# Kernel tuning notes

Measured on AMD Instinct MI355X. Metric: run time of the kernel, lower is better.

## Reference

```python
import jax, jax.numpy as jnp
import numpy as np

B, S, D, F = 8, 4096, 512, 4

def setup_inputs() -> dict:
    key = jax.random.key(0)
    k1, k2, k3, k4 = jax.random.split(key, 4)
    return {
        "inputs": jax.random.normal(k1, (B, S, D), dtype=jnp.float32),
        "values": jax.random.normal(k2, (B, S, F * D), dtype=jnp.float32),
        "W_out": jax.random.normal(k3, (2 * D, D), dtype=jnp.float32) * 0.02,
        "w_score": jax.random.normal(k4, (D, 1), dtype=jnp.float32) * 0.02,
        "b_score": jnp.zeros((1,), dtype=jnp.float32),
        "n": F,
    }

def reference(inputs, values, W_out, w_score, b_score, n):
    # inputs: [B,S,D]; values: [B,S,F*D] -> per-position lattice factors [B,S,F,D]
    b, s, d = inputs.shape
    f = values.shape[2] // d
    mem = values.reshape(b, s, f, d)
    # dot-attention of each position's query over its F factor vectors
    scores = jnp.einsum('bsd,bsfd->bsf', inputs, mem)  # [B,S,F]
    valid = jnp.arange(f) < n                          # lattice mask from n
    scores = jnp.where(valid, scores, jnp.float32(-1e9))
    attn = jax.nn.softmax(scores, axis=-1)
    ctx = jnp.einsum('bsf,bsfd->bsd', attn, mem)       # [B,S,D]
    # OpenNMT GlobalAttention (dot): tanh(linear_out([ctx; q])), no bias
    cat = jnp.concatenate([ctx, inputs], axis=-1)      # [B,S,2D]
    attn_h = jnp.tanh(cat @ W_out)                     # [B,S,D]
    # sigmoid context gate from the query
    gate = jax.nn.sigmoid(inputs @ w_score + b_score)  # [B,S,1]
    # dropout is identity in eval; residual add
    return attn_h * gate + inputs
```

## Files before the change

### kernel.cpp

```cpp
#include <hip/hip_runtime.h>
#include <hip/hip_bf16.h>
#include <math.h>

#define BATCH 8
#define SEQ   4096
#define DIM   512
#define FDIM  4
#define M_TOTAL (BATCH*SEQ)
#define K_TOTAL (2*DIM)
#define N_TOTAL DIM

#define PRE_BLOCKS (M_TOTAL/4)
#define WCONV_BLOCKS ((K_TOTAL/64)*(N_TOTAL/64))

typedef __bf16 bf16x8 __attribute__((ext_vector_type(8)));
typedef float  f32x4  __attribute__((ext_vector_type(4)));

__device__ __forceinline__ void gload_lds16(const void* g, void* l) {
    __builtin_amdgcn_global_load_lds(
        (__attribute__((address_space(1))) void*)(void*)g,
        (__attribute__((address_space(3))) void*)l,
        16, 0, 0);
}

__device__ __forceinline__ float dot4(float4 a, float4 b) {
    return a.x*b.x + a.y*b.y + a.z*b.z + a.w*b.w;
}

__device__ __forceinline__ void store_bf4(__hip_bfloat16* dst, float4 v) {
    __hip_bfloat16 t[4];
    t[0] = __float2bfloat16(v.x); t[1] = __float2bfloat16(v.y);
    t[2] = __float2bfloat16(v.z); t[3] = __float2bfloat16(v.w);
    *reinterpret_cast<uint2*>(dst) = *reinterpret_cast<const uint2*>(t);
}

__device__ __forceinline__ float fast_tanh(float x) {
    float e = __expf(2.f * x);
    return 1.f - 2.f * __builtin_amdgcn_rcpf(e + 1.f);
}

__global__ __launch_bounds__(256)
void pre_kernel(const float* __restrict__ inputs,
                const float* __restrict__ values,
                const float* __restrict__ W,
                const float* __restrict__ w_score,
                const float* __restrict__ b_score,
                const int*   __restrict__ n_ptr,
                __hip_bfloat16* __restrict__ cat,
                float* __restrict__ gate,
                __hip_bfloat16* __restrict__ Wt)
{
    __shared__ float ws[64][65];

    const int tid  = threadIdx.x;

    if (blockIdx.x >= PRE_BLOCKS) {
        const int t  = blockIdx.x - PRE_BLOCKS;
        const int k0 = (t & 15) * 64;
        const int n0 = (t >> 4) * 64;
        #pragma unroll
        for (int i = 0; i < 16; ++i) {
            int e = i * 256 + tid;
            int r = e >> 6, c = e & 63;
            ws[r][c] = W[(size_t)(k0 + r) * N_TOTAL + n0 + c];
        }
        __syncthreads();
        #pragma unroll
        for (int i = 0; i < 16; ++i) {
            int e = i * 256 + tid;
            int nr = e >> 6, kc = e & 63;
            Wt[(size_t)(n0 + nr) * K_TOTAL + k0 + kc] = __float2bfloat16(ws[kc][nr]);
        }
        return;
    }

    const int lane = tid & 63;
    const int wv   = tid >> 6;
    const int p    = blockIdx.x * 4 + wv;

    const float4* qg = (const float4*)(inputs + (size_t)p * DIM);
    float4 qa = qg[lane], qb = qg[lane + 64];

    const float4* vg = (const float4*)(values + (size_t)p * (FDIM*DIM));
    float4 ma[4], mb[4];
    float s[4];
    #pragma unroll
    for (int f = 0; f < 4; ++f) {
        ma[f] = vg[f * 128 + lane];
        mb[f] = vg[f * 128 + lane + 64];
        s[f] = dot4(qa, ma[f]) + dot4(qb, mb[f]);
    }
    const float4* wg = (const float4*)w_score;
    float g = dot4(qa, wg[lane]) + dot4(qb, wg[lane + 64]);

    #pragma unroll
    for (int off = 1; off < 64; off <<= 1) {
        s[0] += __shfl_xor(s[0], off, 64);
        s[1] += __shfl_xor(s[1], off, 64);
        s[2] += __shfl_xor(s[2], off, 64);
        s[3] += __shfl_xor(s[3], off, 64);
        g    += __shfl_xor(g,    off, 64);
    }

    const int nv = *n_ptr;
    #pragma unroll
    for (int f = 0; f < 4; ++f) if (f >= nv) s[f] = -1e9f;
    float mx = fmaxf(fmaxf(s[0], s[1]), fmaxf(s[2], s[3]));
    float e0 = __expf(s[0] - mx), e1 = __expf(s[1] - mx);
    float e2 = __expf(s[2] - mx), e3 = __expf(s[3] - mx);
    float inv = __builtin_amdgcn_rcpf(e0 + e1 + e2 + e3);
    float a[4] = { e0 * inv, e1 * inv, e2 * inv, e3 * inv };

    float4 ca = {0.f, 0.f, 0.f, 0.f}, cb = {0.f, 0.f, 0.f, 0.f};
    #pragma unroll
    for (int f = 0; f < 4; ++f) {
        ca.x += a[f] * ma[f].x; ca.y += a[f] * ma[f].y;
        ca.z += a[f] * ma[f].z; ca.w += a[f] * ma[f].w;
        cb.x += a[f] * mb[f].x; cb.y += a[f] * mb[f].y;
        cb.z += a[f] * mb[f].z; cb.w += a[f] * mb[f].w;
    }

    __hip_bfloat16* cp = cat + (size_t)p * K_TOTAL;
    store_bf4(cp +        4 * lane, ca);
    store_bf4(cp + 256  + 4 * lane, cb);
    store_bf4(cp + 512  + 4 * lane, qa);
    store_bf4(cp + 768  + 4 * lane, qb);

    if (lane == 0) {
        float t = g + b_score[0];
        gate[p] = __builtin_amdgcn_rcpf(1.f + __expf(-t));
    }
}

__global__ __launch_bounds__(256)
void gemm_ep(const __hip_bfloat16* __restrict__ A,
             const __hip_bfloat16* __restrict__ Bt,
             const float* __restrict__ gate,
             const float* __restrict__ inputs,
             float* __restrict__ out)
{
    __shared__ __align__(16) __hip_bfloat16 As[128 * 64];
    __shared__ __align__(16) __hip_bfloat16 Bs[128 * 64];

    const int tid  = threadIdx.x;
    const int bm   = blockIdx.x;
    const int bn   = blockIdx.y;
    const int wid  = tid >> 6;
    const int lane = tid & 63;
    const int wr   = wid >> 1;
    const int wc   = wid & 1;
    const int la   = lane & 15;
    const int lb   = lane >> 4;

    const int K = K_TOTAL;
    const __hip_bfloat16* Ag = A  + (size_t)(bm * 128) * K;
    const __hip_bfloat16* Bg = Bt + (size_t)(bn * 128) * K;

    f32x4 acc[4][4] = {};

    for (int kt = 0; kt < K; kt += 64) {
        __syncthreads();
        #pragma unroll
        for (int ps = 0; ps < 4; ++ps) {
            int cl  = ps * 256 + tid;
            int row = cl >> 3;
            int c   = cl & 7;
            int sc_ = c ^ (row & 7);
            gload_lds16(Ag + (size_t)row * K + kt + sc_ * 8, As + cl * 8);
            gload_lds16(Bg + (size_t)row * K + kt + sc_ * 8, Bs + cl * 8);
        }
        __syncthreads();

        #pragma unroll
        for (int kk = 0; kk < 2; ++kk) {
            bf16x8 af[4], bfv[4];
            #pragma unroll
            for (int i = 0; i < 4; ++i) {
                int row = wr * 64 + i * 16 + la;
                int c   = (kk * 4 + lb) ^ (row & 7);
                af[i] = *reinterpret_cast<const bf16x8*>(As + row * 64 + c * 8);
            }
            #pragma unroll
            for (int j = 0; j < 4; ++j) {
                int row = wc * 64 + j * 16 + la;
                int c   = (kk * 4 + lb) ^ (row & 7);
                bfv[j] = *reinterpret_cast<const bf16x8*>(Bs + row * 64 + c * 8);
            }
            #pragma unroll
            for (int i = 0; i < 4; ++i)
                #pragma unroll
                for (int j = 0; j < 4; ++j)
                    acc[i][j] = __builtin_amdgcn_mfma_f32_16x16x32_bf16(af[i], bfv[j], acc[i][j], 0, 0, 0);
        }
    }

    const int row0 = bm * 128 + wr * 64;
    const int col0 = bn * 128 + wc * 64;
    #pragma unroll
    for (int i = 0; i < 4; ++i) {
        #pragma unroll
        for (int j = 0; j < 4; ++j) {
            const int col = col0 + j * 16 + la;
            const int rb  = row0 + i * 16 + lb * 4;
            #pragma unroll
            for (int r = 0; r < 4; ++r) {
                const int row = rb + r;
                float v = fast_tanh(acc[i][j][r]) * gate[row] + inputs[(size_t)row * DIM + col];
                out[(size_t)row * DIM + col] = v;
            }
        }
    }
}

extern "C" void kernel_launch(void* const* d_in, const int* in_sizes, int n_in,
                              void* d_out, int out_size, void* d_ws, size_t ws_size,
                              hipStream_t stream) {
    const float* inputs  = (const float*)d_in[0];
    const float* values  = (const float*)d_in[1];
    const float* W_out   = (const float*)d_in[2];
    const float* w_score = (const float*)d_in[3];
    const float* b_score = (const float*)d_in[4];
    const int*   n_ptr   = (const int*)d_in[5];
    float* out = (float*)d_out;

    char* ws = (char*)d_ws;
    __hip_bfloat16* cat  = (__hip_bfloat16*)ws;
    float*          gate = (float*)(ws + (size_t)M_TOTAL * K_TOTAL * 2);
    __hip_bfloat16* Wt   = (__hip_bfloat16*)(ws + (size_t)M_TOTAL * K_TOTAL * 2
                                                + (size_t)M_TOTAL * 4);

    pre_kernel<<<PRE_BLOCKS + WCONV_BLOCKS, 256, 0, stream>>>(
        inputs, values, W_out, w_score, b_score, n_ptr, cat, gate, Wt);
    dim3 g3(M_TOTAL / 128, N_TOTAL / 128);
    gemm_ep<<<g3, 256, 0, stream>>>(cat, Wt, gate, inputs, out);
}
```

Measured before the change: 135.3 us.

## Stop materializing query half of cat; convert fp32 inputs to bf16 inside GEMM

The pre-kernel now writes only the bf16 context (half the previous buffer) instead of the full [ctx; q] concatenation. For the second half of K, the GEMM loads fp32 inputs directly, converts them to bf16 in registers and stores them into the swizzled LDS tile. This removes a write and re-read of the query half, but the GEMM now reads fp32 (twice the bytes) through synchronous register loads rather than async global_load_lds, and each input tile is re-read by the four N-blocks. Launch bounds also add a min-blocks hint of 4.

```diff
diff --git a/kernel.cpp b/kernel.cpp
--- a/kernel.cpp
+++ b/kernel.cpp
@@ -46,7 +46,7 @@
                 const float* __restrict__ w_score,
                 const float* __restrict__ b_score,
                 const int*   __restrict__ n_ptr,
-                __hip_bfloat16* __restrict__ cat,
+                __hip_bfloat16* __restrict__ ctx,
                 float* __restrict__ gate,
                 __hip_bfloat16* __restrict__ Wt)
 {
@@ -120,11 +120,9 @@
         cb.z += a[f] * mb[f].z; cb.w += a[f] * mb[f].w;
     }
 
-    __hip_bfloat16* cp = cat + (size_t)p * K_TOTAL;
+    __hip_bfloat16* cp = ctx + (size_t)p * DIM;
     store_bf4(cp +        4 * lane, ca);
     store_bf4(cp + 256  + 4 * lane, cb);
-    store_bf4(cp + 512  + 4 * lane, qa);
-    store_bf4(cp + 768  + 4 * lane, qb);
 
     if (lane == 0) {
         float t = g + b_score[0];
@@ -132,8 +130,8 @@
     }
 }
 
-__global__ __launch_bounds__(256)
-void gemm_ep(const __hip_bfloat16* __restrict__ A,
+__global__ __launch_bounds__(256, 4)
+void gemm_ep(const __hip_bfloat16* __restrict__ Actx,
              const __hip_bfloat16* __restrict__ Bt,
              const float* __restrict__ gate,
              const float* __restrict__ inputs,
@@ -152,22 +150,42 @@
     const int la   = lane & 15;
     const int lb   = lane >> 4;
 
-    const int K = K_TOTAL;
-    const __hip_bfloat16* Ag = A  + (size_t)(bm * 128) * K;
-    const __hip_bfloat16* Bg = Bt + (size_t)(bn * 128) * K;
+    const __hip_bfloat16* Ag = Actx + (size_t)(bm * 128) * DIM;
+    const float*          Qg = inputs + (size_t)(bm * 128) * DIM;
+    const __hip_bfloat16* Bg = Bt + (size_t)(bn * 128) * K_TOTAL;
 
     f32x4 acc[4][4] = {};
 
-    for (int kt = 0; kt < K; kt += 64) {
+    for (int kt = 0; kt < K_TOTAL; kt += 64) {
         __syncthreads();
-        #pragma unroll
-        for (int ps = 0; ps < 4; ++ps) {
-            int cl  = ps * 256 + tid;
-            int row = cl >> 3;
-            int c   = cl & 7;
-            int sc_ = c ^ (row & 7);
-            gload_lds16(Ag + (size_t)row * K + kt + sc_ * 8, As + cl * 8);
-            gload_lds16(Bg + (size_t)row * K + kt + sc_ * 8, Bs + cl * 8);
+        if (kt < 512) {
+            #pragma unroll
+            for (int ps = 0; ps < 4; ++ps) {
+                int cl  = ps * 256 + tid;
+                int row = cl >> 3;
+                int c   = cl & 7;
+                int sc_ = c ^ (row & 7);
+                gload_lds16(Ag + (size_t)row * DIM + kt + sc_ * 8, As + cl * 8);
+                gload_lds16(Bg + (size_t)row * K_TOTAL + kt + sc_ * 8, Bs + cl * 8);
+            }
+        } else {
+            #pragma unroll
+            for (int ps = 0; ps < 4; ++ps) {
+                int cl  = ps * 256 + tid;
+                int row = cl >> 3;
+                int c   = cl & 7;
+                int sc_ = c ^ (row & 7);
+                gload_lds16(Bg + (size_t)row * K_TOTAL + kt + sc_ * 8, Bs + cl * 8);
+                const float* src = Qg + (size_t)row * DIM + (kt - 512) + sc_ * 8;
+                float4 f0 = ((const float4*)src)[0];
+                float4 f1 = ((const float4*)src)[1];
+                __hip_bfloat16 t[8];
+                t[0] = __float2bfloat16(f0.x); t[1] = __float2bfloat16(f0.y);
+                t[2] = __float2bfloat16(f0.z); t[3] = __float2bfloat16(f0.w);
+                t[4] = __float2bfloat16(f1.x); t[5] = __float2bfloat16(f1.y);
+                t[6] = __float2bfloat16(f1.z); t[7] = __float2bfloat16(f1.w);
+                *reinterpret_cast<uint4*>(As + cl * 8) = *reinterpret_cast<const uint4*>(t);
+            }
         }
         __syncthreads();
 
@@ -224,13 +242,13 @@
     float* out = (float*)d_out;
 
     char* ws = (char*)d_ws;
-    __hip_bfloat16* cat  = (__hip_bfloat16*)ws;
-    float*          gate = (float*)(ws + (size_t)M_TOTAL * K_TOTAL * 2);
-    __hip_bfloat16* Wt   = (__hip_bfloat16*)(ws + (size_t)M_TOTAL * K_TOTAL * 2
+    __hip_bfloat16* ctx  = (__hip_bfloat16*)ws;
+    float*          gate = (float*)(ws + (size_t)M_TOTAL * DIM * 2);
+    __hip_bfloat16* Wt   = (__hip_bfloat16*)(ws + (size_t)M_TOTAL * DIM * 2
                                                 + (size_t)M_TOTAL * 4);
 
     pre_kernel<<<PRE_BLOCKS + WCONV_BLOCKS, 256, 0, stream>>>(
-        inputs, values, W_out, w_score, b_score, n_ptr, cat, gate, Wt);
+        inputs, values, W_out, w_score, b_score, n_ptr, ctx, gate, Wt);
     dim3 g3(M_TOTAL / 128, N_TOTAL / 128);
-    gemm_ep<<<g3, 256, 0, stream>>>(cat, Wt, gate, inputs, out);
-}
+    gemm_ep<<<g3, 256, 0, stream>>>(ctx, Wt, gate, inputs, out);
+}
```

Result: faster. 126.9 us (-6.2%).

## Enlarge GEMM tiles to 256x256 with double-buffered LDS and bf16 residual

Applied to the files above, without the earlier changes.

The GEMM now uses 256x256 tiles with 512 threads and double-buffers its LDS stages, so global-to-LDS loads overlap the MFMA work through manual waitcnt and barriers. Block indices are swizzled for better L2 locality, and gate values are cached in LDS. The residual now reads the bf16 copy of the query from the cat buffer instead of the fp32 inputs, which cuts epilogue bandwidth but adds bf16 rounding error to the residual term. Larger tiles give fewer blocks (256), which may reduce occupancy and raise register pressure.

```diff
diff --git a/kernel.cpp b/kernel.cpp
--- a/kernel.cpp
+++ b/kernel.cpp
@@ -12,6 +12,11 @@
 
 #define PRE_BLOCKS (M_TOTAL/4)
 #define WCONV_BLOCKS ((K_TOTAL/64)*(N_TOTAL/64))
+
+#define BM 256
+#define BN 256
+#define BK 64
+#define NKT (K_TOTAL/BK)
 
 typedef __bf16 bf16x8 __attribute__((ext_vector_type(8)));
 typedef float  f32x4  __attribute__((ext_vector_type(4)));
@@ -132,72 +137,96 @@
     }
 }
 
-__global__ __launch_bounds__(256)
+__global__ __launch_bounds__(512, 2)
 void gemm_ep(const __hip_bfloat16* __restrict__ A,
              const __hip_bfloat16* __restrict__ Bt,
              const float* __restrict__ gate,
-             const float* __restrict__ inputs,
              float* __restrict__ out)
 {
-    __shared__ __align__(16) __hip_bfloat16 As[128 * 64];
-    __shared__ __align__(16) __hip_bfloat16 Bs[128 * 64];
-
-    const int tid  = threadIdx.x;
-    const int bm   = blockIdx.x;
-    const int bn   = blockIdx.y;
+    __shared__ __align__(16) __hip_bfloat16 As[2][BM * BK];
+    __shared__ __align__(16) __hip_bfloat16 Bs[2][BN * BK];
+    __shared__ float gateLds[BM];
+
+    const int tid = threadIdx.x;
+    const int logical = (blockIdx.x & 7) * 32 + (blockIdx.x >> 3);
+    const int bm = logical >> 1;
+    const int bn = logical & 1;
+
     const int wid  = tid >> 6;
     const int lane = tid & 63;
-    const int wr   = wid >> 1;
-    const int wc   = wid & 1;
+    const int wr   = wid & 1;
+    const int wc   = wid >> 1;
     const int la   = lane & 15;
     const int lb   = lane >> 4;
 
-    const int K = K_TOTAL;
-    const __hip_bfloat16* Ag = A  + (size_t)(bm * 128) * K;
-    const __hip_bfloat16* Bg = Bt + (size_t)(bn * 128) * K;
-
-    f32x4 acc[4][4] = {};
-
-    for (int kt = 0; kt < K; kt += 64) {
-        __syncthreads();
+    const __hip_bfloat16* Ag = A  + (size_t)(bm * BM) * K_TOTAL;
+    const __hip_bfloat16* Bg = Bt + (size_t)(bn * BN) * K_TOTAL;
+
+    if (tid < BM) gateLds[tid] = gate[bm * BM + tid];
+    __syncthreads();
+
+    auto STAGE = [&](int t, int buf) {
+        const int kt = t * BK;
         #pragma unroll
         for (int ps = 0; ps < 4; ++ps) {
-            int cl  = ps * 256 + tid;
+            int cl  = ps * 512 + tid;
             int row = cl >> 3;
             int c   = cl & 7;
-            int sc_ = c ^ (row & 7);
-            gload_lds16(Ag + (size_t)row * K + kt + sc_ * 8, As + cl * 8);
-            gload_lds16(Bg + (size_t)row * K + kt + sc_ * 8, Bs + cl * 8);
-        }
-        __syncthreads();
-
+            int sc  = c ^ (row & 7);
+            gload_lds16(Ag + (size_t)row * K_TOTAL + kt + sc * 8, &As[buf][cl * 8]);
+            gload_lds16(Bg + (size_t)row * K_TOTAL + kt + sc * 8, &Bs[buf][cl * 8]);
+        }
+    };
+
+    f32x4 acc[8][4] = {};
+
+    auto COMPUTE = [&](int buf) {
         #pragma unroll
         for (int kk = 0; kk < 2; ++kk) {
-            bf16x8 af[4], bfv[4];
-            #pragma unroll
-            for (int i = 0; i < 4; ++i) {
-                int row = wr * 64 + i * 16 + la;
-                int c   = (kk * 4 + lb) ^ (row & 7);
-                af[i] = *reinterpret_cast<const bf16x8*>(As + row * 64 + c * 8);
+            bf16x8 af[8], bfv[4];
+            #pragma unroll
+            for (int i = 0; i < 8; ++i) {
+                int row = wr * 128 + i * 16 + la;
+                int cc  = (kk * 4 + lb) ^ (row & 7);
+                af[i] = *reinterpret_cast<const bf16x8*>(&As[buf][row * BK + cc * 8]);
             }
             #pragma unroll
             for (int j = 0; j < 4; ++j) {
                 int row = wc * 64 + j * 16 + la;
-                int c   = (kk * 4 + lb) ^ (row & 7);
-                bfv[j] = *reinterpret_cast<const bf16x8*>(Bs + row * 64 + c * 8);
+                int cc  = (kk * 4 + lb) ^ (row & 7);
+                bfv[j] = *reinterpret_cast<const bf16x8*>(&Bs[buf][row * BK + cc * 8]);
             }
             #pragma unroll
-            for (int i = 0; i < 4; ++i)
+            for (int i = 0; i < 8; ++i)
                 #pragma unroll
                 for (int j = 0; j < 4; ++j)
                     acc[i][j] = __builtin_amdgcn_mfma_f32_16x16x32_bf16(af[i], bfv[j], acc[i][j], 0, 0, 0);
         }
-    }
-
-    const int row0 = bm * 128 + wr * 64;
-    const int col0 = bn * 128 + wc * 64;
-    #pragma unroll
-    for (int i = 0; i < 4; ++i) {
+    };
+
+    STAGE(0, 0);
+    STAGE(1, 1);
+
+    #pragma unroll 2
+    for (int t = 0; t < NKT - 2; ++t) {
+        asm volatile("s_waitcnt vmcnt(8)" ::: "memory");
+        __builtin_amdgcn_s_barrier();
+        COMPUTE(t & 1);
+        asm volatile("s_waitcnt lgkmcnt(0)" ::: "memory");
+        __builtin_amdgcn_s_barrier();
+        STAGE(t + 2, t & 1);
+    }
+    asm volatile("s_waitcnt vmcnt(8)" ::: "memory");
+    __builtin_amdgcn_s_barrier();
+    COMPUTE(0);
+    asm volatile("s_waitcnt vmcnt(0)" ::: "memory");
+    __builtin_amdgcn_s_barrier();
+    COMPUTE(1);
+
+    const int row0 = bm * BM + wr * 128;
+    const int col0 = bn * BN + wc * 64;
+    #pragma unroll
+    for (int i = 0; i < 8; ++i) {
         #pragma unroll
         for (int j = 0; j < 4; ++j) {
             const int col = col0 + j * 16 + la;
@@ -205,7 +234,8 @@
             #pragma unroll
             for (int r = 0; r < 4; ++r) {
                 const int row = rb + r;
-                float v = fast_tanh(acc[i][j][r]) * gate[row] + inputs[(size_t)row * DIM + col];
+                float q = __bfloat162float(A[(size_t)row * K_TOTAL + 512 + col]);
+                float v = fast_tanh(acc[i][j][r]) * gateLds[row - bm * BM] + q;
                 out[(size_t)row * DIM + col] = v;
             }
         }
@@ -231,6 +261,5 @@
 
     pre_kernel<<<PRE_BLOCKS + WCONV_BLOCKS, 256, 0, stream>>>(
         inputs, values, W_out, w_score, b_score, n_ptr, cat, gate, Wt);
-    dim3 g3(M_TOTAL / 128, N_TOTAL / 128);
-    gemm_ep<<<g3, 256, 0, stream>>>(cat, Wt, gate, inputs, out);
-}
+    gemm_ep<<<(M_TOTAL / BM) * (N_TOTAL / BN), 512, 0, stream>>>(cat, Wt, gate, out);
+}
```

After: 140.9 us. +4.2%, slower.

## Fuse attention preprocessing into GEMM with per-block LDS cat tile

Applied to the files above, without the earlier changes.

Each block computes softmax context, gate and the bf16 concatenated row tile for 32 positions directly into swizzled LDS, then runs the MFMA GEMM over the full N=512 against the transposed weight read from global/L2 with register double-buffering. The epilogue takes the residual from the LDS copy of the query. This removes the global cat/gate workspace round trip and the separate inputs reread. In exchange, every block streams the whole weight matrix from L2, and the residual is rounded to bf16.

```diff
diff --git a/kernel.cpp b/kernel.cpp
--- a/kernel.cpp
+++ b/kernel.cpp
@@ -10,18 +10,12 @@
 #define K_TOTAL (2*DIM)
 #define N_TOTAL DIM
 
-#define PRE_BLOCKS (M_TOTAL/4)
+#define MB 32
+#define FUSED_BLOCKS (M_TOTAL/MB)
 #define WCONV_BLOCKS ((K_TOTAL/64)*(N_TOTAL/64))
 
 typedef __bf16 bf16x8 __attribute__((ext_vector_type(8)));
 typedef float  f32x4  __attribute__((ext_vector_type(4)));
-
-__device__ __forceinline__ void gload_lds16(const void* g, void* l) {
-    __builtin_amdgcn_global_load_lds(
-        (__attribute__((address_space(1))) void*)(void*)g,
-        (__attribute__((address_space(3))) void*)l,
-        16, 0, 0);
-}
 
 __device__ __forceinline__ float dot4(float4 a, float4 b) {
     return a.x*b.x + a.y*b.y + a.z*b.z + a.w*b.w;
@@ -40,176 +34,170 @@
 }
 
 __global__ __launch_bounds__(256)
-void pre_kernel(const float* __restrict__ inputs,
-                const float* __restrict__ values,
-                const float* __restrict__ W,
-                const float* __restrict__ w_score,
-                const float* __restrict__ b_score,
-                const int*   __restrict__ n_ptr,
-                __hip_bfloat16* __restrict__ cat,
-                float* __restrict__ gate,
-                __hip_bfloat16* __restrict__ Wt)
+void wconv(const float* __restrict__ W, __hip_bfloat16* __restrict__ Wt)
 {
     __shared__ float ws[64][65];
+    const int tid = threadIdx.x;
+    const int t  = blockIdx.x;
+    const int k0 = (t & 15) * 64;
+    const int n0 = (t >> 4) * 64;
+    #pragma unroll
+    for (int i = 0; i < 16; ++i) {
+        int e = i * 256 + tid;
+        int r = e >> 6, c = e & 63;
+        ws[r][c] = W[(size_t)(k0 + r) * N_TOTAL + n0 + c];
+    }
+    __syncthreads();
+    #pragma unroll
+    for (int i = 0; i < 16; ++i) {
+        int e = i * 256 + tid;
+        int nr = e >> 6, kc = e & 63;
+        Wt[(size_t)(n0 + nr) * K_TOTAL + k0 + kc] = __float2bfloat16(ws[kc][nr]);
+    }
+}
+
+__device__ __forceinline__ void cat_store4(__hip_bfloat16* catL, int row, int k, float4 v) {
+    int ck   = k >> 3;
+    int phys = ck ^ (row & 7);
+    char* dst = (char*)catL + row * 2048 + (phys << 4) + ((k & 7) << 1);
+    store_bf4((__hip_bfloat16*)dst, v);
+}
+
+__global__ __launch_bounds__(256, 2)
+void fused_kernel(const float* __restrict__ inputs,
+                  const float* __restrict__ values,
+                  const __hip_bfloat16* __restrict__ Bt,
+                  const float* __restrict__ w_score,
+                  const float* __restrict__ b_score,
+                  const int*   __restrict__ n_ptr,
+                  float* __restrict__ out)
+{
+    __shared__ __align__(16) __hip_bfloat16 catL[MB * K_TOTAL];
+    __shared__ float gateL[MB];
 
     const int tid  = threadIdx.x;
-
-    if (blockIdx.x >= PRE_BLOCKS) {
-        const int t  = blockIdx.x - PRE_BLOCKS;
-        const int k0 = (t & 15) * 64;
-        const int n0 = (t >> 4) * 64;
-        #pragma unroll
-        for (int i = 0; i < 16; ++i) {
-            int e = i * 256 + tid;
-            int r = e >> 6, c = e & 63;
-            ws[r][c] = W[(size_t)(k0 + r) * N_TOTAL + n0 + c];
-        }
-        __syncthreads();
-        #pragma unroll
-        for (int i = 0; i < 16; ++i) {
-            int e = i * 256 + tid;
-            int nr = e >> 6, kc = e & 63;
-            Wt[(size_t)(n0 + nr) * K_TOTAL + k0 + kc] = __float2bfloat16(ws[kc][nr]);
-        }
-        return;
-    }
-
     const int lane = tid & 63;
     const int wv   = tid >> 6;
-    const int p    = blockIdx.x * 4 + wv;
-
-    const float4* qg = (const float4*)(inputs + (size_t)p * DIM);
-    float4 qa = qg[lane], qb = qg[lane + 64];
-
-    const float4* vg = (const float4*)(values + (size_t)p * (FDIM*DIM));
-    float4 ma[4], mb[4];
-    float s[4];
-    #pragma unroll
-    for (int f = 0; f < 4; ++f) {
-        ma[f] = vg[f * 128 + lane];
-        mb[f] = vg[f * 128 + lane + 64];
-        s[f] = dot4(qa, ma[f]) + dot4(qb, mb[f]);
-    }
+    const int bp   = blockIdx.x * MB;
+    const int nv   = *n_ptr;
+
     const float4* wg = (const float4*)w_score;
-    float g = dot4(qa, wg[lane]) + dot4(qb, wg[lane + 64]);
-
-    #pragma unroll
-    for (int off = 1; off < 64; off <<= 1) {
-        s[0] += __shfl_xor(s[0], off, 64);
-        s[1] += __shfl_xor(s[1], off, 64);
-        s[2] += __shfl_xor(s[2], off, 64);
-        s[3] += __shfl_xor(s[3], off, 64);
-        g    += __shfl_xor(g,    off, 64);
-    }
-
-    const int nv = *n_ptr;
-    #pragma unroll
-    for (int f = 0; f < 4; ++f) if (f >= nv) s[f] = -1e9f;
-    float mx = fmaxf(fmaxf(s[0], s[1]), fmaxf(s[2], s[3]));
-    float e0 = __expf(s[0] - mx), e1 = __expf(s[1] - mx);
-    float e2 = __expf(s[2] - mx), e3 = __expf(s[3] - mx);
-    float inv = __builtin_amdgcn_rcpf(e0 + e1 + e2 + e3);
-    float a[4] = { e0 * inv, e1 * inv, e2 * inv, e3 * inv };
-
-    float4 ca = {0.f, 0.f, 0.f, 0.f}, cb = {0.f, 0.f, 0.f, 0.f};
-    #pragma unroll
-    for (int f = 0; f < 4; ++f) {
-        ca.x += a[f] * ma[f].x; ca.y += a[f] * ma[f].y;
-        ca.z += a[f] * ma[f].z; ca.w += a[f] * ma[f].w;
-        cb.x += a[f] * mb[f].x; cb.y += a[f] * mb[f].y;
-        cb.z += a[f] * mb[f].z; cb.w += a[f] * mb[f].w;
-    }
-
-    __hip_bfloat16* cp = cat + (size_t)p * K_TOTAL;
-    store_bf4(cp +        4 * lane, ca);
-    store_bf4(cp + 256  + 4 * lane, cb);
-    store_bf4(cp + 512  + 4 * lane, qa);
-    store_bf4(cp + 768  + 4 * lane, qb);
-
-    if (lane == 0) {
-        float t = g + b_score[0];
-        gate[p] = __builtin_amdgcn_rcpf(1.f + __expf(-t));
-    }
-}
-
-__global__ __launch_bounds__(256)
-void gemm_ep(const __hip_bfloat16* __restrict__ A,
-             const __hip_bfloat16* __restrict__ Bt,
-             const float* __restrict__ gate,
-             const float* __restrict__ inputs,
-             float* __restrict__ out)
-{
-    __shared__ __align__(16) __hip_bfloat16 As[128 * 64];
-    __shared__ __align__(16) __hip_bfloat16 Bs[128 * 64];
-
-    const int tid  = threadIdx.x;
-    const int bm   = blockIdx.x;
-    const int bn   = blockIdx.y;
-    const int wid  = tid >> 6;
-    const int lane = tid & 63;
-    const int wr   = wid >> 1;
-    const int wc   = wid & 1;
-    const int la   = lane & 15;
-    const int lb   = lane >> 4;
-
-    const int K = K_TOTAL;
-    const __hip_bfloat16* Ag = A  + (size_t)(bm * 128) * K;
-    const __hip_bfloat16* Bg = Bt + (size_t)(bn * 128) * K;
-
-    f32x4 acc[4][4] = {};
-
-    for (int kt = 0; kt < K; kt += 64) {
-        __syncthreads();
-        #pragma unroll
-        for (int ps = 0; ps < 4; ++ps) {
-            int cl  = ps * 256 + tid;
-            int row = cl >> 3;
-            int c   = cl & 7;
-            int sc_ = c ^ (row & 7);
-            gload_lds16(Ag + (size_t)row * K + kt + sc_ * 8, As + cl * 8);
-            gload_lds16(Bg + (size_t)row * K + kt + sc_ * 8, Bs + cl * 8);
-        }
-        __syncthreads();
-
-        #pragma unroll
-        for (int kk = 0; kk < 2; ++kk) {
-            bf16x8 af[4], bfv[4];
-            #pragma unroll
-            for (int i = 0; i < 4; ++i) {
-                int row = wr * 64 + i * 16 + la;
-                int c   = (kk * 4 + lb) ^ (row & 7);
-                af[i] = *reinterpret_cast<const bf16x8*>(As + row * 64 + c * 8);
-            }
-            #pragma unroll
-            for (int j = 0; j < 4; ++j) {
-                int row = wc * 64 + j * 16 + la;
-                int c   = (kk * 4 + lb) ^ (row & 7);
-                bfv[j] = *reinterpret_cast<const bf16x8*>(Bs + row * 64 + c * 8);
-            }
-            #pragma unroll
-            for (int i = 0; i < 4; ++i)
-                #pragma unroll
-                for (int j = 0; j < 4; ++j)
-                    acc[i][j] = __builtin_amdgcn_mfma_f32_16x16x32_bf16(af[i], bfv[j], acc[i][j], 0, 0, 0);
-        }
-    }
-
-    const int row0 = bm * 128 + wr * 64;
-    const int col0 = bn * 128 + wc * 64;
-    #pragma unroll
-    for (int i = 0; i < 4; ++i) {
-        #pragma unroll
-        for (int j = 0; j < 4; ++j) {
-            const int col = col0 + j * 16 + la;
-            const int rb  = row0 + i * 16 + lb * 4;
+    #pragma unroll 2
+    for (int it = 0; it < MB / 4; ++it) {
+        const int p = wv * (MB / 4) + it;
+        const float4* qg = (const float4*)(inputs + (size_t)(bp + p) * DIM);
+        float4 qa = qg[lane], qb = qg[lane + 64];
+
+        const float4* vg = (const float4*)(values + (size_t)(bp + p) * (FDIM*DIM));
+        float4 ma[4], mb[4];
+        float s[4];
+        #pragma unroll
+        for (int f = 0; f < 4; ++f) {
+            ma[f] = vg[f * 128 + lane];
+            mb[f] = vg[f * 128 + lane + 64];
+            s[f] = dot4(qa, ma[f]) + dot4(qb, mb[f]);
+        }
+        float g = dot4(qa, wg[lane]) + dot4(qb, wg[lane + 64]);
+
+        #pragma unroll
+        for (int off = 1; off < 64; off <<= 1) {
+            s[0] += __shfl_xor(s[0], off, 64);
+            s[1] += __shfl_xor(s[1], off, 64);
+            s[2] += __shfl_xor(s[2], off, 64);
+            s[3] += __shfl_xor(s[3], off, 64);
+            g    += __shfl_xor(g,    off, 64);
+        }
+
+        #pragma unroll
+        for (int f = 0; f < 4; ++f) if (f >= nv) s[f] = -1e9f;
+        float mx = fmaxf(fmaxf(s[0], s[1]), fmaxf(s[2], s[3]));
+        float e0 = __expf(s[0] - mx), e1 = __expf(s[1] - mx);
+        float e2 = __expf(s[2] - mx), e3 = __expf(s[3] - mx);
+        float inv = __builtin_amdgcn_rcpf(e0 + e1 + e2 + e3);
+        float a0 = e0*inv, a1 = e1*inv, a2 = e2*inv, a3 = e3*inv;
+
+        float4 ca, cb;
+        ca.x = a0*ma[0].x + a1*ma[1].x + a2*ma[2].x + a3*ma[3].x;
+        ca.y = a0*ma[0].y + a1*ma[1].y + a2*ma[2].y + a3*ma[3].y;
+        ca.z = a0*ma[0].z + a1*ma[1].z + a2*ma[2].z + a3*ma[3].z;
+        ca.w = a0*ma[0].w + a1*ma[1].w + a2*ma[2].w + a3*ma[3].w;
+        cb.x = a0*mb[0].x + a1*mb[1].x + a2*mb[2].x + a3*mb[3].x;
+        cb.y = a0*mb[0].y + a1*mb[1].y + a2*mb[2].y + a3*mb[3].y;
+        cb.z = a0*mb[0].z + a1*mb[1].z + a2*mb[2].z + a3*mb[3].z;
+        cb.w = a0*mb[0].w + a1*mb[1].w + a2*mb[2].w + a3*mb[3].w;
+
+        cat_store4(catL, p,         lane * 4, ca);
+        cat_store4(catL, p, 256  +  lane * 4, cb);
+        cat_store4(catL, p, 512  +  lane * 4, qa);
+        cat_store4(catL, p, 768  +  lane * 4, qb);
+
+        if (lane == 0) {
+            float t = g + b_score[0];
+            gateL[p] = __builtin_amdgcn_rcpf(1.f + __expf(-t));
+        }
+    }
+    __syncthreads();
+
+    const int la = lane & 15;
+    const int lb = lane >> 4;
+    const int nw = wv * 128;
+
+    f32x4 acc[2][8] = {};
+
+#define LOADSTEP(af, bf, kt, kk) do {                                         \
+        int ck0 = (kt) * 8 + (kk) * 4 + lb;                                   \
+        _Pragma("unroll")                                                     \
+        for (int m = 0; m < 2; ++m) {                                         \
+            int row = m * 16 + la;                                            \
+            af[m] = *reinterpret_cast<const bf16x8*>(                         \
+                (const char*)catL + row * 2048 + ((ck0 ^ (row & 7)) << 4));   \
+        }                                                                     \
+        _Pragma("unroll")                                                     \
+        for (int j = 0; j < 8; ++j) {                                         \
+            int nrow = nw + j * 16 + la;                                      \
+            bf[j] = *reinterpret_cast<const bf16x8*>(                         \
+                Bt + (size_t)nrow * K_TOTAL + (kt) * 64 + (kk) * 32 + lb * 8);\
+        }                                                                     \
+    } while (0)
+
+#define MFMASTEP(af, bf) do {                                                 \
+        _Pragma("unroll")                                                     \
+        for (int m = 0; m < 2; ++m)                                           \
+            _Pragma("unroll")                                                 \
+            for (int j = 0; j < 8; ++j)                                       \
+                acc[m][j] = __builtin_amdgcn_mfma_f32_16x16x32_bf16(          \
+                    af[m], bf[j], acc[m][j], 0, 0, 0);                        \
+    } while (0)
+
+    bf16x8 aA[2], bA[8], aB[2], bB[8];
+    LOADSTEP(aA, bA, 0, 0);
+    #pragma unroll
+    for (int s = 0; s < 31; ++s) {
+        const int ns = s + 1, nkt = ns >> 1, nkk = ns & 1;
+        if ((s & 1) == 0) { LOADSTEP(aB, bB, nkt, nkk); MFMASTEP(aA, bA); }
+        else              { LOADSTEP(aA, bA, nkt, nkk); MFMASTEP(aB, bB); }
+    }
+    MFMASTEP(aB, bB);
+
+    #pragma unroll
+    for (int m = 0; m < 2; ++m) {
+        #pragma unroll
+        for (int j = 0; j < 8; ++j) {
+            const int col = nw + j * 16 + la;
+            const int ckq = 64 + (col >> 3);
             #pragma unroll
             for (int r = 0; r < 4; ++r) {
-                const int row = rb + r;
-                float v = fast_tanh(acc[i][j][r]) * gate[row] + inputs[(size_t)row * DIM + col];
-                out[(size_t)row * DIM + col] = v;
+                const int row = m * 16 + lb * 4 + r;
+                float q = __bfloat162float(*(const __hip_bfloat16*)(
+                    (const char*)catL + row * 2048 + ((ckq ^ (row & 7)) << 4)
+                    + ((col & 7) << 1)));
+                float v = fast_tanh(acc[m][j][r]) * gateL[row] + q;
+                out[(size_t)(bp + row) * DIM + col] = v;
             }
         }
     }
+#undef LOADSTEP
+#undef MFMASTEP
 }
 
 extern "C" void kernel_launch(void* const* d_in, const int* in_sizes, int n_in,
@@ -223,14 +211,9 @@
     const int*   n_ptr   = (const int*)d_in[5];
     float* out = (float*)d_out;
 
-    char* ws = (char*)d_ws;
-    __hip_bfloat16* cat  = (__hip_bfloat16*)ws;
-    float*          gate = (float*)(ws + (size_t)M_TOTAL * K_TOTAL * 2);
-    __hip_bfloat16* Wt   = (__hip_bfloat16*)(ws + (size_t)M_TOTAL * K_TOTAL * 2
-                                                + (size_t)M_TOTAL * 4);
-
-    pre_kernel<<<PRE_BLOCKS + WCONV_BLOCKS, 256, 0, stream>>>(
-        inputs, values, W_out, w_score, b_score, n_ptr, cat, gate, Wt);
-    dim3 g3(M_TOTAL / 128, N_TOTAL / 128);
-    gemm_ep<<<g3, 256, 0, stream>>>(cat, Wt, gate, inputs, out);
-}
+    __hip_bfloat16* Wt = (__hip_bfloat16*)d_ws;
+
+    wconv<<<WCONV_BLOCKS, 256, 0, stream>>>(W_out, Wt);
+    fused_kernel<<<FUSED_BLOCKS, 256, 0, stream>>>(
+        inputs, values, Wt, w_score, b_score, n_ptr, out);
+}
```

Result: slower. 189.2 us (+39.8%).
